# Kernel tuning notes

Measured on AMD Instinct MI355X. Metric: run time of the kernel, lower is better.

## Reference

```python
import jax, jax.numpy as jnp
import numpy as np

NUM_LAYERS = 3
IN_C, HID_C, OUT_C = 128, 128, 64
N_NODES, N_EDGES = 100000, 1600000


def setup_inputs() -> dict:
    key = jax.random.key(0)
    ks = jax.random.split(key, 8)
    x = jax.random.normal(ks[0], (N_NODES, IN_C), dtype=jnp.float32)
    edge_index = jax.random.randint(ks[1], (2, N_EDGES), 0, N_NODES, dtype=jnp.int64)
    s_in = 1.0 / np.sqrt(IN_C)
    s_h = 1.0 / np.sqrt(HID_C)
    W_in = jax.random.uniform(ks[2], (IN_C, HID_C), jnp.float32, -s_in, s_in)
    W_convs = jax.random.uniform(ks[3], (NUM_LAYERS, HID_C, HID_C), jnp.float32, -s_h, s_h)
    b_convs = jax.random.uniform(ks[4], (NUM_LAYERS, HID_C), jnp.float32, -s_h, s_h)
    W_fc = jax.random.uniform(ks[5], (HID_C, OUT_C), jnp.float32, -s_h, s_h)
    b_fc = jax.random.uniform(ks[6], (OUT_C,), jnp.float32, -s_h, s_h)
    return {"x": x, "edge_index": edge_index, "W_in": W_in, "W_convs": W_convs,
            "b_convs": b_convs, "W_fc": W_fc, "b_fc": b_fc}


def _g2_tau(x_new, row, col, num_nodes):
    # per-edge squared L2 difference of gated features (p=2)
    d = x_new[row] - x_new[col]            # [E, H]
    diffs = jnp.sum(d * d, axis=-1)        # [E]
    tau_vals = jax.ops.segment_sum(diffs, row, num_segments=num_nodes)
    deg = jax.ops.segment_sum(jnp.ones_like(diffs), row, num_segments=num_nodes) + 1e-10
    return jnp.tanh(tau_vals / deg)[:, None]  # [N, 1]


def reference(x, edge_index, W_in, W_convs, b_convs, W_fc, b_fc):
    row, col = edge_index[0], edge_index[1]
    n = x.shape[0]
    x = x @ W_in                                            # input_fc (no bias)
    for l in range(NUM_LAYERS):
        h = x @ W_convs[l]                                  # GCNConv linear
        agg = jax.ops.segment_sum(h[row], col, num_segments=n) + b_convs[l]
        x_new = jax.nn.relu(agg)
        tau = _g2_tau(x_new, row, col, n)
        x = (1.0 - tau) * x + tau * x_new
    return x @ W_fc + b_fc
```

## Files before the change

kernel.cpp:

```cpp
#include <hip/hip_runtime.h>
#include <hip/hip_bf16.h>

#define N_NODES 100000
#define N_EDGES 1600000
#define HID 128
#define OUTC 64
#define NLAYERS 3

#define M_PAD 100032
#define SCAN_N (2 * N_NODES)
#define SCAN_B 1024
#define SCAN_NB ((SCAN_N + SCAN_B - 1) / SCAN_B)

typedef __attribute__((ext_vector_type(8))) short short8;
typedef __attribute__((ext_vector_type(4))) float f32x4;
typedef __attribute__((ext_vector_type(2))) float f32x2;

__device__ __forceinline__ unsigned short f2b(float f) {
  return __builtin_bit_cast(unsigned short, __float2bfloat16(f));
}
__device__ __forceinline__ float blo(unsigned int u) {
  return __builtin_bit_cast(float, u << 16);
}
__device__ __forceinline__ float bhi(unsigned int u) {
  return __builtin_bit_cast(float, u & 0xffff0000u);
}

__global__ __launch_bounds__(128) void cast_w_kernel(
    const float* __restrict__ W_in, const float* __restrict__ W_convs,
    const float* __restrict__ W_fc, unsigned short* __restrict__ wt) {
  const int b = blockIdx.x;
  const int k = threadIdx.x;
  const float* src;
  unsigned short* dst;
  int n, N;
  if (b < 128) {
    n = b; N = 128; src = W_in; dst = wt + n * 128;
  } else if (b < 512) {
    const int l = (b - 128) >> 7;
    n = (b - 128) & 127; N = 128;
    src = W_convs + (size_t)l * 16384;
    dst = wt + 16384 * (1 + l) + n * 128;
  } else {
    n = b - 512; N = 64; src = W_fc; dst = wt + 65536 + n * 128;
  }
  dst[k] = f2b(src[k * N + n]);
}

template <int MODE>
__global__ __launch_bounds__(256) void gemm_mfma_kernel(
    const float* __restrict__ Xf, const unsigned short* __restrict__ Xb,
    const unsigned short* __restrict__ Wt, const float* __restrict__ bias,
    float* __restrict__ Y, unsigned short* __restrict__ Yb) {
  constexpr int NT = (MODE == 2) ? 4 : 8;
  const int wave = threadIdx.x >> 6;
  const int lane = threadIdx.x & 63;
  const int row0 = blockIdx.x * 64 + wave * 16;
  const int lm = lane & 15;
  const int lk = (lane >> 4) * 8;

  f32x4 acc[NT];
#pragma unroll
  for (int t = 0; t < NT; ++t) acc[t] = {0.f, 0.f, 0.f, 0.f};

  const int arow = row0 + lm;
#pragma unroll
  for (int ki = 0; ki < 4; ++ki) {
    short8 a;
    if (MODE == 0) {
      float av[8];
      const bool ok = arow < N_NODES;
#pragma unroll
      for (int j = 0; j < 8; ++j)
        av[j] = ok ? Xf[(size_t)arow * 128 + ki * 32 + lk + j] : 0.f;
#pragma unroll
      for (int j = 0; j < 8; ++j)
        a[j] = (short)f2b(av[j]);
    } else {
      a = *reinterpret_cast<const short8*>(Xb + (size_t)arow * 128 + ki * 32 + lk);
    }
#pragma unroll
    for (int t = 0; t < NT; ++t) {
      const short8 b =
          *reinterpret_cast<const short8*>(Wt + (t * 16 + lm) * 128 + ki * 32 + lk);
      acc[t] = __builtin_amdgcn_mfma_f32_16x16x32_bf16(a, b, acc[t], 0, 0, 0);
    }
  }

  const int orow = row0 + (lane >> 4) * 4;
#pragma unroll
  for (int t = 0; t < NT; ++t) {
#pragma unroll
    for (int r = 0; r < 4; ++r) {
      const int rr = orow + r;
      const int cc = t * 16 + lm;
      const float v = acc[t][r];
      if (MODE == 2) {
        if (rr < N_NODES) Y[(size_t)rr * OUTC + cc] = v + bias[cc];
      } else {
        Yb[(size_t)rr * 128 + cc] = f2b(v);
      }
    }
  }
}

__global__ __launch_bounds__(256) void count_kernel(
    const int* __restrict__ row, const int* __restrict__ col,
    int* __restrict__ counts, unsigned int* __restrict__ ranks) {
  const int e = blockIdx.x * 256 + threadIdx.x;
  if (e >= N_EDGES) return;
  const int pr = atomicAdd(counts + row[e], 1);
  const int pc = atomicAdd(counts + N_NODES + col[e], 1);
  ranks[e] = (unsigned)pr | ((unsigned)pc << 16);
}

__global__ __launch_bounds__(SCAN_B) void scan1_kernel(
    const int* __restrict__ counts, int* __restrict__ incl,
    int* __restrict__ bsum) {
  __shared__ int tmp[SCAN_B];
  const int i = blockIdx.x * SCAN_B + threadIdx.x;
  tmp[threadIdx.x] = (i < SCAN_N) ? counts[i] : 0;
  __syncthreads();
  for (int d = 1; d < SCAN_B; d <<= 1) {
    int t = (threadIdx.x >= d) ? tmp[threadIdx.x - d] : 0;
    __syncthreads();
    tmp[threadIdx.x] += t;
    __syncthreads();
  }
  if (i < SCAN_N) incl[i] = tmp[threadIdx.x];
  if (threadIdx.x == SCAN_B - 1) bsum[blockIdx.x] = tmp[SCAN_B - 1];
}

__global__ __launch_bounds__(256) void scan2_kernel(int* __restrict__ bsum) {
  __shared__ int tmp[256];
  tmp[threadIdx.x] = (threadIdx.x < SCAN_NB) ? bsum[threadIdx.x] : 0;
  __syncthreads();
  for (int d = 1; d < 256; d <<= 1) {
    int t = (threadIdx.x >= d) ? tmp[threadIdx.x - d] : 0;
    __syncthreads();
    tmp[threadIdx.x] += t;
    __syncthreads();
  }
  if (threadIdx.x < SCAN_NB) bsum[threadIdx.x] = tmp[threadIdx.x];
}

__global__ __launch_bounds__(SCAN_B) void scan3_kernel(
    const int* __restrict__ counts, const int* __restrict__ incl,
    const int* __restrict__ bsum, int2* __restrict__ seg) {
  const int i = blockIdx.x * SCAN_B + threadIdx.x;
  if (i >= SCAN_N) return;
  const int c = counts[i];
  const int v = incl[i] + (blockIdx.x > 0 ? bsum[blockIdx.x - 1] : 0);
  seg[i] = make_int2(v - c, c);
}

__global__ __launch_bounds__(256) void fill_kernel(
    const int* __restrict__ row, const int* __restrict__ col,
    const unsigned int* __restrict__ ranks, const int2* __restrict__ seg,
    int* __restrict__ adj) {
  const int p = blockIdx.x * 256 + threadIdx.x;
  if (p * 2 >= N_EDGES) return;
  const int2 r2 = reinterpret_cast<const int2*>(row)[p];
  const int2 c2 = reinterpret_cast<const int2*>(col)[p];
  const uint2 u2 = reinterpret_cast<const uint2*>(ranks)[p];
  adj[seg[r2.x].x + (int)(u2.x & 0xffffu)] = c2.x;
  adj[seg[N_NODES + c2.x].x + (int)(u2.x >> 16)] = r2.x;
  adj[seg[r2.y].x + (int)(u2.y & 0xffffu)] = c2.y;
  adj[seg[N_NODES + c2.y].x + (int)(u2.y >> 16)] = r2.y;
}

__global__ __launch_bounds__(256) void aggregate_kernel(
    const unsigned int* __restrict__ hb, const int2* __restrict__ seg,
    const int* __restrict__ adj, const float* __restrict__ b,
    unsigned int* __restrict__ xnewb, unsigned short* __restrict__ xnew8) {
  const int g = blockIdx.x * 256 + threadIdx.x;
  const int n = g >> 6;
  if (n >= N_NODES) return;
  const int lane = g & 63;
  const int2 sg = seg[N_NODES + n];
  const int start = sg.x;
  const int end = sg.x + sg.y;

  float a0x = 0.f, a0y = 0.f, a1x = 0.f, a1y = 0.f;
  float a2x = 0.f, a2y = 0.f, a3x = 0.f, a3y = 0.f;
  int i = start;
  for (; i + 3 < end; i += 4) {
    const unsigned int v0 = hb[(size_t)adj[i] * 64 + lane];
    const unsigned int v1 = hb[(size_t)adj[i + 1] * 64 + lane];
    const unsigned int v2 = hb[(size_t)adj[i + 2] * 64 + lane];
    const unsigned int v3 = hb[(size_t)adj[i + 3] * 64 + lane];
    a0x += blo(v0); a0y += bhi(v0);
    a1x += blo(v1); a1y += bhi(v1);
    a2x += blo(v2); a2y += bhi(v2);
    a3x += blo(v3); a3y += bhi(v3);
  }
  for (; i < end; ++i) {
    const unsigned int v0 = hb[(size_t)adj[i] * 64 + lane];
    a0x += blo(v0); a0y += bhi(v0);
  }
  const float2 bb = *reinterpret_cast<const float2*>(b + lane * 2);
  const float ox = fmaxf(((a0x + a1x) + (a2x + a3x)) + bb.x, 0.f);
  const float oy = fmaxf(((a0y + a1y) + (a2y + a3y)) + bb.y, 0.f);
  xnewb[(size_t)n * 64 + lane] = (unsigned)f2b(ox) | ((unsigned)f2b(oy) << 16);
  const unsigned int p8 = __builtin_amdgcn_cvt_pk_fp8_f32(ox, oy, 0u, false);
  xnew8[(size_t)n * 64 + lane] = (unsigned short)(p8 & 0xffffu);
}

__global__ __launch_bounds__(256) void tau_update_kernel(
    const unsigned int* __restrict__ xnewb, const unsigned short* __restrict__ xnew8,
    const int2* __restrict__ seg, const int* __restrict__ adj,
    unsigned int* __restrict__ x) {
  const int g = blockIdx.x * 256 + threadIdx.x;
  const int n = g >> 6;
  if (n >= N_NODES) return;
  const int lane = g & 63;
  const int2 sg = seg[n];
  const int start = sg.x;
  const int cnt = sg.y;
  const int end = start + cnt;

  const unsigned int mp = xnewb[(size_t)n * 64 + lane];
  const float mx = blo(mp), my = bhi(mp);

  float s0 = 0.f, s1 = 0.f, s2 = 0.f, s3 = 0.f;
  int i = start;
  for (; i + 3 < end; i += 4) {
    const unsigned int u0 = xnew8[(size_t)adj[i] * 64 + lane];
    const unsigned int u1 = xnew8[(size_t)adj[i + 1] * 64 + lane];
    const unsigned int u2 = xnew8[(size_t)adj[i + 2] * 64 + lane];
    const unsigned int u3 = xnew8[(size_t)adj[i + 3] * 64 + lane];
    const f32x2 v0 = __builtin_amdgcn_cvt_pk_f32_fp8(u0, false);
    const f32x2 v1 = __builtin_amdgcn_cvt_pk_f32_fp8(u1, false);
    const f32x2 v2 = __builtin_amdgcn_cvt_pk_f32_fp8(u2, false);
    const f32x2 v3 = __builtin_amdgcn_cvt_pk_f32_fp8(u3, false);
    const float d0x = mx - v0[0], d0y = my - v0[1];
    const float d1x = mx - v1[0], d1y = my - v1[1];
    const float d2x = mx - v2[0], d2y = my - v2[1];
    const float d3x = mx - v3[0], d3y = my - v3[1];
    s0 += d0x * d0x + d0y * d0y;
    s1 += d1x * d1x + d1y * d1y;
    s2 += d2x * d2x + d2y * d2y;
    s3 += d3x * d3x + d3y * d3y;
  }
  for (; i < end; ++i) {
    const unsigned int u0 = xnew8[(size_t)adj[i] * 64 + lane];
    const f32x2 v0 = __builtin_amdgcn_cvt_pk_f32_fp8(u0, false);
    const float d0x = mx - v0[0], d0y = my - v0[1];
    s0 += d0x * d0x + d0y * d0y;
  }
  float s = (s0 + s1) + (s2 + s3);
  s += __shfl_xor(s, 1);
  s += __shfl_xor(s, 2);
  s += __shfl_xor(s, 4);
  s += __shfl_xor(s, 8);
  s += __shfl_xor(s, 16);
  s += __shfl_xor(s, 32);
  const float tau = tanhf(s / ((float)cnt + 1e-10f));

  const unsigned int xp = x[(size_t)n * 64 + lane];
  const float nx = (1.f - tau) * blo(xp) + tau * mx;
  const float ny = (1.f - tau) * bhi(xp) + tau * my;
  x[(size_t)n * 64 + lane] = (unsigned)f2b(nx) | ((unsigned)f2b(ny) << 16);
}

extern "C" void kernel_launch(void* const* d_in, const int* in_sizes, int n_in,
                              void* d_out, int out_size, void* d_ws,
                              size_t ws_size, hipStream_t stream) {
  const float* x_in = (const float*)d_in[0];
  const int* ei = (const int*)d_in[1];
  const float* W_in = (const float*)d_in[2];
  const float* W_convs = (const float*)d_in[3];
  const float* b_convs = (const float*)d_in[4];
  const float* W_fc = (const float*)d_in[5];
  const float* b_fc = (const float*)d_in[6];
  float* out = (float*)d_out;

  const int* row = ei;
  const int* col = ei + N_EDGES;

  const size_t PF = (size_t)M_PAD * HID;
  unsigned short* xb2 = (unsigned short*)d_ws;
  unsigned short* hb = xb2 + PF;
  unsigned short* xnewb = hb + PF;
  unsigned short* xnew8 = xnewb + PF;
  unsigned short* wt = xnew8 + (size_t)N_NODES * 64;
  int* counts = (int*)(wt + 73728);
  int* incl = counts + SCAN_N;
  int* bsum = incl + SCAN_N;
  int2* seg = (int2*)(bsum + 1024);
  unsigned int* ranks = (unsigned int*)(seg + SCAN_N);
  int* adj = (int*)(ranks + N_EDGES);

  const int GEMM_BLOCKS = M_PAD / 64;
  const int EDGE_BLOCKS = (N_EDGES + 255) / 256;
  const int PAIR_BLOCKS = (N_EDGES / 2 + 255) / 256;
  const int WAVE_BLOCKS = (N_NODES * 64 + 255) / 256;

  cast_w_kernel<<<576, 128, 0, stream>>>(W_in, W_convs, W_fc, wt);

  hipMemsetAsync(counts, 0, SCAN_N * sizeof(int), stream);
  count_kernel<<<EDGE_BLOCKS, 256, 0, stream>>>(row, col, counts, ranks);
  scan1_kernel<<<SCAN_NB, SCAN_B, 0, stream>>>(counts, incl, bsum);
  scan2_kernel<<<1, 256, 0, stream>>>(bsum);
  scan3_kernel<<<SCAN_NB, SCAN_B, 0, stream>>>(counts, incl, bsum, seg);
  fill_kernel<<<PAIR_BLOCKS, 256, 0, stream>>>(row, col, ranks, seg, adj);

  gemm_mfma_kernel<0><<<GEMM_BLOCKS, 256, 0, stream>>>(
      x_in, nullptr, wt, nullptr, nullptr, xb2);

  for (int l = 0; l < NLAYERS; ++l) {
    const unsigned short* wtl = wt + 16384 * (1 + l);
    const float* bl = b_convs + (size_t)l * HID;

    gemm_mfma_kernel<1><<<GEMM_BLOCKS, 256, 0, stream>>>(
        nullptr, xb2, wtl, nullptr, nullptr, hb);
    aggregate_kernel<<<WAVE_BLOCKS, 256, 0, stream>>>(
        (const unsigned int*)hb, seg, adj, bl, (unsigned int*)xnewb, xnew8);
    tau_update_kernel<<<WAVE_BLOCKS, 256, 0, stream>>>(
        (const unsigned int*)xnewb, xnew8, seg, adj, (unsigned int*)xb2);
  }

  gemm_mfma_kernel<2><<<GEMM_BLOCKS, 256, 0, stream>>>(
      nullptr, xb2, wt + 65536, b_fc, out, nullptr);
}
```

Before: 838.4 us.

## Fuse tau update with following layer GEMM and widen aggregate unroll

The tau/gated-update kernel now writes its updated bf16 rows into a swizzled LDS tile and runs the next layer's MFMA GEMM (or the final FC with bias) in the same kernel. This removes a separate GEMM launch per layer and the global re-read of x. The aggregate kernel's gather loop also goes from 4 to 8 independent loads in flight. In exchange, the fused kernel processes 16 nodes sequentially per wave at 64 nodes per block, which lowers parallelism for the latency-bound tau gather compared with one node per wave across many blocks.

```diff
diff --git a/kernel.cpp b/kernel.cpp
--- a/kernel.cpp
+++ b/kernel.cpp
@@ -50,9 +50,8 @@
 template <int MODE>
 __global__ __launch_bounds__(256) void gemm_mfma_kernel(
     const float* __restrict__ Xf, const unsigned short* __restrict__ Xb,
-    const unsigned short* __restrict__ Wt, const float* __restrict__ bias,
-    float* __restrict__ Y, unsigned short* __restrict__ Yb) {
-  constexpr int NT = (MODE == 2) ? 4 : 8;
+    const unsigned short* __restrict__ Wt, unsigned short* __restrict__ Yb) {
+  constexpr int NT = 8;
   const int wave = threadIdx.x >> 6;
   const int lane = threadIdx.x & 63;
   const int row0 = blockIdx.x * 64 + wave * 16;
@@ -92,14 +91,7 @@
   for (int t = 0; t < NT; ++t) {
 #pragma unroll
     for (int r = 0; r < 4; ++r) {
-      const int rr = orow + r;
-      const int cc = t * 16 + lm;
-      const float v = acc[t][r];
-      if (MODE == 2) {
-        if (rr < N_NODES) Y[(size_t)rr * OUTC + cc] = v + bias[cc];
-      } else {
-        Yb[(size_t)rr * 128 + cc] = f2b(v);
-      }
+      Yb[(size_t)(orow + r) * 128 + t * 16 + lm] = f2b(acc[t][r]);
     }
   }
 }
@@ -181,86 +173,137 @@
   const int start = sg.x;
   const int end = sg.x + sg.y;
 
-  float a0x = 0.f, a0y = 0.f, a1x = 0.f, a1y = 0.f;
-  float a2x = 0.f, a2y = 0.f, a3x = 0.f, a3y = 0.f;
+  float ax[8], ay[8];
+#pragma unroll
+  for (int j = 0; j < 8; ++j) { ax[j] = 0.f; ay[j] = 0.f; }
   int i = start;
-  for (; i + 3 < end; i += 4) {
-    const unsigned int v0 = hb[(size_t)adj[i] * 64 + lane];
-    const unsigned int v1 = hb[(size_t)adj[i + 1] * 64 + lane];
-    const unsigned int v2 = hb[(size_t)adj[i + 2] * 64 + lane];
-    const unsigned int v3 = hb[(size_t)adj[i + 3] * 64 + lane];
-    a0x += blo(v0); a0y += bhi(v0);
-    a1x += blo(v1); a1y += bhi(v1);
-    a2x += blo(v2); a2y += bhi(v2);
-    a3x += blo(v3); a3y += bhi(v3);
+  for (; i + 7 < end; i += 8) {
+    unsigned int v[8];
+#pragma unroll
+    for (int j = 0; j < 8; ++j) v[j] = hb[(size_t)adj[i + j] * 64 + lane];
+#pragma unroll
+    for (int j = 0; j < 8; ++j) { ax[j] += blo(v[j]); ay[j] += bhi(v[j]); }
   }
   for (; i < end; ++i) {
     const unsigned int v0 = hb[(size_t)adj[i] * 64 + lane];
-    a0x += blo(v0); a0y += bhi(v0);
-  }
+    ax[0] += blo(v0); ay[0] += bhi(v0);
+  }
+#pragma unroll
+  for (int j = 4; j < 8; ++j) { ax[j - 4] += ax[j]; ay[j - 4] += ay[j]; }
   const float2 bb = *reinterpret_cast<const float2*>(b + lane * 2);
-  const float ox = fmaxf(((a0x + a1x) + (a2x + a3x)) + bb.x, 0.f);
-  const float oy = fmaxf(((a0y + a1y) + (a2y + a3y)) + bb.y, 0.f);
+  const float ox = fmaxf(((ax[0] + ax[1]) + (ax[2] + ax[3])) + bb.x, 0.f);
+  const float oy = fmaxf(((ay[0] + ay[1]) + (ay[2] + ay[3])) + bb.y, 0.f);
   xnewb[(size_t)n * 64 + lane] = (unsigned)f2b(ox) | ((unsigned)f2b(oy) << 16);
   const unsigned int p8 = __builtin_amdgcn_cvt_pk_fp8_f32(ox, oy, 0u, false);
   xnew8[(size_t)n * 64 + lane] = (unsigned short)(p8 & 0xffffu);
 }
 
-__global__ __launch_bounds__(256) void tau_update_kernel(
+template <int OUT_MODE>
+__global__ __launch_bounds__(256) void taugemm_kernel(
     const unsigned int* __restrict__ xnewb, const unsigned short* __restrict__ xnew8,
     const int2* __restrict__ seg, const int* __restrict__ adj,
-    unsigned int* __restrict__ x) {
-  const int g = blockIdx.x * 256 + threadIdx.x;
-  const int n = g >> 6;
-  if (n >= N_NODES) return;
-  const int lane = g & 63;
-  const int2 sg = seg[n];
-  const int start = sg.x;
-  const int cnt = sg.y;
-  const int end = start + cnt;
-
-  const unsigned int mp = xnewb[(size_t)n * 64 + lane];
-  const float mx = blo(mp), my = bhi(mp);
-
-  float s0 = 0.f, s1 = 0.f, s2 = 0.f, s3 = 0.f;
-  int i = start;
-  for (; i + 3 < end; i += 4) {
-    const unsigned int u0 = xnew8[(size_t)adj[i] * 64 + lane];
-    const unsigned int u1 = xnew8[(size_t)adj[i + 1] * 64 + lane];
-    const unsigned int u2 = xnew8[(size_t)adj[i + 2] * 64 + lane];
-    const unsigned int u3 = xnew8[(size_t)adj[i + 3] * 64 + lane];
-    const f32x2 v0 = __builtin_amdgcn_cvt_pk_f32_fp8(u0, false);
-    const f32x2 v1 = __builtin_amdgcn_cvt_pk_f32_fp8(u1, false);
-    const f32x2 v2 = __builtin_amdgcn_cvt_pk_f32_fp8(u2, false);
-    const f32x2 v3 = __builtin_amdgcn_cvt_pk_f32_fp8(u3, false);
-    const float d0x = mx - v0[0], d0y = my - v0[1];
-    const float d1x = mx - v1[0], d1y = my - v1[1];
-    const float d2x = mx - v2[0], d2y = my - v2[1];
-    const float d3x = mx - v3[0], d3y = my - v3[1];
-    s0 += d0x * d0x + d0y * d0y;
-    s1 += d1x * d1x + d1y * d1y;
-    s2 += d2x * d2x + d2y * d2y;
-    s3 += d3x * d3x + d3y * d3y;
-  }
-  for (; i < end; ++i) {
-    const unsigned int u0 = xnew8[(size_t)adj[i] * 64 + lane];
-    const f32x2 v0 = __builtin_amdgcn_cvt_pk_f32_fp8(u0, false);
-    const float d0x = mx - v0[0], d0y = my - v0[1];
-    s0 += d0x * d0x + d0y * d0y;
-  }
-  float s = (s0 + s1) + (s2 + s3);
-  s += __shfl_xor(s, 1);
-  s += __shfl_xor(s, 2);
-  s += __shfl_xor(s, 4);
-  s += __shfl_xor(s, 8);
-  s += __shfl_xor(s, 16);
-  s += __shfl_xor(s, 32);
-  const float tau = tanhf(s / ((float)cnt + 1e-10f));
-
-  const unsigned int xp = x[(size_t)n * 64 + lane];
-  const float nx = (1.f - tau) * blo(xp) + tau * mx;
-  const float ny = (1.f - tau) * bhi(xp) + tau * my;
-  x[(size_t)n * 64 + lane] = (unsigned)f2b(nx) | ((unsigned)f2b(ny) << 16);
+    unsigned int* __restrict__ x, const unsigned short* __restrict__ Wt,
+    const float* __restrict__ bias, unsigned short* __restrict__ Yb,
+    float* __restrict__ Yf) {
+  __shared__ unsigned int lds[64 * 64];
+  const int wave = threadIdx.x >> 6;
+  const int lane = threadIdx.x & 63;
+  const int row0 = blockIdx.x * 64 + wave * 16;
+
+  for (int i = 0; i < 16; ++i) {
+    const int n = row0 + i;
+    unsigned int packed = 0;
+    if (n < N_NODES) {
+      const int2 sg = seg[n];
+      const int start = sg.x;
+      const int cnt = sg.y;
+      const int end = start + cnt;
+
+      const unsigned int mp = xnewb[(size_t)n * 64 + lane];
+      const float mx = blo(mp), my = bhi(mp);
+
+      float s0 = 0.f, s1 = 0.f, s2 = 0.f, s3 = 0.f;
+      int ii = start;
+      for (; ii + 3 < end; ii += 4) {
+        const unsigned int u0 = xnew8[(size_t)adj[ii] * 64 + lane];
+        const unsigned int u1 = xnew8[(size_t)adj[ii + 1] * 64 + lane];
+        const unsigned int u2 = xnew8[(size_t)adj[ii + 2] * 64 + lane];
+        const unsigned int u3 = xnew8[(size_t)adj[ii + 3] * 64 + lane];
+        const f32x2 v0 = __builtin_amdgcn_cvt_pk_f32_fp8(u0, false);
+        const f32x2 v1 = __builtin_amdgcn_cvt_pk_f32_fp8(u1, false);
+        const f32x2 v2 = __builtin_amdgcn_cvt_pk_f32_fp8(u2, false);
+        const f32x2 v3 = __builtin_amdgcn_cvt_pk_f32_fp8(u3, false);
+        const float d0x = mx - v0[0], d0y = my - v0[1];
+        const float d1x = mx - v1[0], d1y = my - v1[1];
+        const float d2x = mx - v2[0], d2y = my - v2[1];
+        const float d3x = mx - v3[0], d3y = my - v3[1];
+        s0 += d0x * d0x + d0y * d0y;
+        s1 += d1x * d1x + d1y * d1y;
+        s2 += d2x * d2x + d2y * d2y;
+        s3 += d3x * d3x + d3y * d3y;
+      }
+      for (; ii < end; ++ii) {
+        const unsigned int u0 = xnew8[(size_t)adj[ii] * 64 + lane];
+        const f32x2 v0 = __builtin_amdgcn_cvt_pk_f32_fp8(u0, false);
+        const float d0x = mx - v0[0], d0y = my - v0[1];
+        s0 += d0x * d0x + d0y * d0y;
+      }
+      float s = (s0 + s1) + (s2 + s3);
+      s += __shfl_xor(s, 1);
+      s += __shfl_xor(s, 2);
+      s += __shfl_xor(s, 4);
+      s += __shfl_xor(s, 8);
+      s += __shfl_xor(s, 16);
+      s += __shfl_xor(s, 32);
+      const float tau = tanhf(s / ((float)cnt + 1e-10f));
+
+      const unsigned int xp = x[(size_t)n * 64 + lane];
+      const float nx = (1.f - tau) * blo(xp) + tau * mx;
+      const float ny = (1.f - tau) * bhi(xp) + tau * my;
+      packed = (unsigned)f2b(nx) | ((unsigned)f2b(ny) << 16);
+      if (OUT_MODE == 0) x[(size_t)n * 64 + lane] = packed;
+    }
+    const int r = wave * 16 + i;
+    const int byte = (r * 256 + lane * 4) ^ ((r & 7) << 4);
+    lds[byte >> 2] = packed;
+  }
+  __syncthreads();
+
+  constexpr int NT = (OUT_MODE == 1) ? 4 : 8;
+  const int lm = lane & 15;
+  const int lk = (lane >> 4) * 8;
+  f32x4 acc[NT];
+#pragma unroll
+  for (int t = 0; t < NT; ++t) acc[t] = {0.f, 0.f, 0.f, 0.f};
+
+  const int ar = wave * 16 + lm;
+#pragma unroll
+  for (int ki = 0; ki < 4; ++ki) {
+    const int abyte = (ar * 256 + ki * 64 + lk * 2) ^ ((ar & 7) << 4);
+    const short8 a = *reinterpret_cast<const short8*>(
+        reinterpret_cast<const char*>(lds) + abyte);
+#pragma unroll
+    for (int t = 0; t < NT; ++t) {
+      const short8 b =
+          *reinterpret_cast<const short8*>(Wt + (t * 16 + lm) * 128 + ki * 32 + lk);
+      acc[t] = __builtin_amdgcn_mfma_f32_16x16x32_bf16(a, b, acc[t], 0, 0, 0);
+    }
+  }
+
+  const int orow = row0 + (lane >> 4) * 4;
+#pragma unroll
+  for (int t = 0; t < NT; ++t) {
+#pragma unroll
+    for (int r = 0; r < 4; ++r) {
+      const int rr = orow + r;
+      const int cc = t * 16 + lm;
+      if (OUT_MODE == 1) {
+        if (rr < N_NODES) Yf[(size_t)rr * OUTC + cc] = acc[t][r] + bias[cc];
+      } else {
+        Yb[(size_t)rr * 128 + cc] = f2b(acc[t][r]);
+      }
+    }
+  }
 }
 
 extern "C" void kernel_launch(void* const* d_in, const int* in_sizes, int n_in,
@@ -305,21 +348,24 @@
   scan3_kernel<<<SCAN_NB, SCAN_B, 0, stream>>>(counts, incl, bsum, seg);
   fill_kernel<<<PAIR_BLOCKS, 256, 0, stream>>>(row, col, ranks, seg, adj);
 
-  gemm_mfma_kernel<0><<<GEMM_BLOCKS, 256, 0, stream>>>(
-      x_in, nullptr, wt, nullptr, nullptr, xb2);
+  gemm_mfma_kernel<0><<<GEMM_BLOCKS, 256, 0, stream>>>(x_in, nullptr, wt, xb2);
+
+  gemm_mfma_kernel<1><<<GEMM_BLOCKS, 256, 0, stream>>>(nullptr, xb2, wt + 16384, hb);
 
   for (int l = 0; l < NLAYERS; ++l) {
-    const unsigned short* wtl = wt + 16384 * (1 + l);
     const float* bl = b_convs + (size_t)l * HID;
 
-    gemm_mfma_kernel<1><<<GEMM_BLOCKS, 256, 0, stream>>>(
-        nullptr, xb2, wtl, nullptr, nullptr, hb);
     aggregate_kernel<<<WAVE_BLOCKS, 256, 0, stream>>>(
         (const unsigned int*)hb, seg, adj, bl, (unsigned int*)xnewb, xnew8);
-    tau_update_kernel<<<WAVE_BLOCKS, 256, 0, stream>>>(
-        (const unsigned int*)xnewb, xnew8, seg, adj, (unsigned int*)xb2);
-  }
-
-  gemm_mfma_kernel<2><<<GEMM_BLOCKS, 256, 0, stream>>>(
-      nullptr, xb2, wt + 65536, b_fc, out, nullptr);
-}
+
+    if (l < NLAYERS - 1) {
+      taugemm_kernel<0><<<GEMM_BLOCKS, 256, 0, stream>>>(
+          (const unsigned int*)xnewb, xnew8, seg, adj, (unsigned int*)xb2,
+          wt + 16384 * (2 + l), nullptr, hb, nullptr);
+    } else {
+      taugemm_kernel<1><<<GEMM_BLOCKS, 256, 0, stream>>>(
+          (const unsigned int*)xnewb, xnew8, seg, adj, (unsigned int*)xb2,
+          wt + 65536, b_fc, nullptr, out);
+    }
+  }
+}
```

Measured after the change: 989.1 us. 18.0% more time.

## Quantize GEMM output to int8 with per-row scale before gather-aggregate

Applied to the files above, without the earlier changes.

Adds a kernel that quantizes each node's bf16 hidden row to int8 with a per-node absmax scale. The aggregation kernel then gathers the 128-byte int8 rows plus one scale per neighbor instead of 256-byte bf16 rows, and its unroll goes from 4 to 8 independent accumulators. The aim is to halve the bytes moved by the random-access neighbor gather, which dominates the layer cost. In exchange it adds an extra kernel pass and a per-neighbor scale load, and lowers precision, which risks exceeding the tolerance.

```diff
diff --git a/kernel.cpp b/kernel.cpp
--- a/kernel.cpp
+++ b/kernel.cpp
@@ -169,10 +169,35 @@
   adj[seg[N_NODES + c2.y].x + (int)(u2.y >> 16)] = r2.y;
 }
 
+__global__ __launch_bounds__(256) void quant_h_kernel(
+    const unsigned int* __restrict__ hb, unsigned short* __restrict__ h8,
+    float* __restrict__ scl) {
+  const int g = blockIdx.x * 256 + threadIdx.x;
+  const int n = g >> 6;
+  if (n >= N_NODES) return;
+  const int lane = g & 63;
+  const unsigned int p = hb[(size_t)n * 64 + lane];
+  const float x0 = blo(p), x1 = bhi(p);
+  float m = fmaxf(fabsf(x0), fabsf(x1));
+  m = fmaxf(m, __shfl_xor(m, 1));
+  m = fmaxf(m, __shfl_xor(m, 2));
+  m = fmaxf(m, __shfl_xor(m, 4));
+  m = fmaxf(m, __shfl_xor(m, 8));
+  m = fmaxf(m, __shfl_xor(m, 16));
+  m = fmaxf(m, __shfl_xor(m, 32));
+  const float inv = (m > 0.f) ? 127.0f / m : 0.f;
+  if (lane == 0) scl[n] = m * (1.0f / 127.0f);
+  const int q0 = __float2int_rn(x0 * inv);
+  const int q1 = __float2int_rn(x1 * inv);
+  h8[(size_t)n * 64 + lane] =
+      (unsigned short)((q0 & 0xff) | ((q1 & 0xff) << 8));
+}
+
 __global__ __launch_bounds__(256) void aggregate_kernel(
-    const unsigned int* __restrict__ hb, const int2* __restrict__ seg,
-    const int* __restrict__ adj, const float* __restrict__ b,
-    unsigned int* __restrict__ xnewb, unsigned short* __restrict__ xnew8) {
+    const unsigned short* __restrict__ h8, const float* __restrict__ scl,
+    const int2* __restrict__ seg, const int* __restrict__ adj,
+    const float* __restrict__ b, unsigned int* __restrict__ xnewb,
+    unsigned short* __restrict__ xnew8) {
   const int g = blockIdx.x * 256 + threadIdx.x;
   const int n = g >> 6;
   if (n >= N_NODES) return;
@@ -181,26 +206,39 @@
   const int start = sg.x;
   const int end = sg.x + sg.y;
 
-  float a0x = 0.f, a0y = 0.f, a1x = 0.f, a1y = 0.f;
-  float a2x = 0.f, a2y = 0.f, a3x = 0.f, a3y = 0.f;
+  float ax[8], ay[8];
+#pragma unroll
+  for (int j = 0; j < 8; ++j) { ax[j] = 0.f; ay[j] = 0.f; }
   int i = start;
-  for (; i + 3 < end; i += 4) {
-    const unsigned int v0 = hb[(size_t)adj[i] * 64 + lane];
-    const unsigned int v1 = hb[(size_t)adj[i + 1] * 64 + lane];
-    const unsigned int v2 = hb[(size_t)adj[i + 2] * 64 + lane];
-    const unsigned int v3 = hb[(size_t)adj[i + 3] * 64 + lane];
-    a0x += blo(v0); a0y += bhi(v0);
-    a1x += blo(v1); a1y += bhi(v1);
-    a2x += blo(v2); a2y += bhi(v2);
-    a3x += blo(v3); a3y += bhi(v3);
+  for (; i + 7 < end; i += 8) {
+    unsigned int u[8];
+    float s[8];
+#pragma unroll
+    for (int j = 0; j < 8; ++j) {
+      const int nb = adj[i + j];
+      u[j] = h8[(size_t)nb * 64 + lane];
+      s[j] = scl[nb];
+    }
+#pragma unroll
+    for (int j = 0; j < 8; ++j) {
+      const float q0 = (float)(int)(signed char)(u[j] & 0xff);
+      const float q1 = (float)((int)(short)(unsigned short)u[j] >> 8);
+      ax[j] += q0 * s[j];
+      ay[j] += q1 * s[j];
+    }
   }
   for (; i < end; ++i) {
-    const unsigned int v0 = hb[(size_t)adj[i] * 64 + lane];
-    a0x += blo(v0); a0y += bhi(v0);
-  }
+    const int nb = adj[i];
+    const unsigned int u0 = h8[(size_t)nb * 64 + lane];
+    const float s0 = scl[nb];
+    ax[0] += (float)(int)(signed char)(u0 & 0xff) * s0;
+    ay[0] += (float)((int)(short)(unsigned short)u0 >> 8) * s0;
+  }
+#pragma unroll
+  for (int j = 4; j < 8; ++j) { ax[j - 4] += ax[j]; ay[j - 4] += ay[j]; }
   const float2 bb = *reinterpret_cast<const float2*>(b + lane * 2);
-  const float ox = fmaxf(((a0x + a1x) + (a2x + a3x)) + bb.x, 0.f);
-  const float oy = fmaxf(((a0y + a1y) + (a2y + a3y)) + bb.y, 0.f);
+  const float ox = fmaxf(((ax[0] + ax[1]) + (ax[2] + ax[3])) + bb.x, 0.f);
+  const float oy = fmaxf(((ay[0] + ay[1]) + (ay[2] + ay[3])) + bb.y, 0.f);
   xnewb[(size_t)n * 64 + lane] = (unsigned)f2b(ox) | ((unsigned)f2b(oy) << 16);
   const unsigned int p8 = __builtin_amdgcn_cvt_pk_fp8_f32(ox, oy, 0u, false);
   xnew8[(size_t)n * 64 + lane] = (unsigned short)(p8 & 0xffffu);
@@ -283,7 +321,9 @@
   unsigned short* hb = xb2 + PF;
   unsigned short* xnewb = hb + PF;
   unsigned short* xnew8 = xnewb + PF;
-  unsigned short* wt = xnew8 + (size_t)N_NODES * 64;
+  unsigned short* h8 = xnew8 + (size_t)N_NODES * 64;
+  float* scl = (float*)(h8 + (size_t)N_NODES * 64);
+  unsigned short* wt = (unsigned short*)(scl + N_NODES);
   int* counts = (int*)(wt + 73728);
   int* incl = counts + SCAN_N;
   int* bsum = incl + SCAN_N;
@@ -314,8 +354,10 @@
 
     gemm_mfma_kernel<1><<<GEMM_BLOCKS, 256, 0, stream>>>(
         nullptr, xb2, wtl, nullptr, nullptr, hb);
+    quant_h_kernel<<<WAVE_BLOCKS, 256, 0, stream>>>(
+        (const unsigned int*)hb, h8, scl);
     aggregate_kernel<<<WAVE_BLOCKS, 256, 0, stream>>>(
-        (const unsigned int*)hb, seg, adj, bl, (unsigned int*)xnewb, xnew8);
+        h8, scl, seg, adj, bl, (unsigned int*)xnewb, xnew8);
     tau_update_kernel<<<WAVE_BLOCKS, 256, 0, stream>>>(
         (const unsigned int*)xnewb, xnew8, seg, adj, (unsigned int*)xb2);
   }
```

After: 836.2 us. About the same (-0.3%).
